# Kernel optimization log

Measured on AMD Instinct MI355X. Metric: run time of the kernel, lower is better.

The kernel has to match this reference:

```python
import jax, jax.numpy as jnp
import numpy as np

POOL = 2  # pool_size from init_kwargs


def setup_inputs() -> dict:
    key = jax.random.key(0)
    b, n = 8192, 64
    A = jax.random.normal(key, (b, n, n), dtype=jnp.float32)
    # SPD construction: A A^T / n + I  (well-conditioned, distinct eigvals a.s.)
    X = A @ jnp.swapaxes(A, -1, -2) / n + jnp.eye(n, dtype=jnp.float32)
    return {"X": X}


def _logm_spd(X):
    # matrix log of batched SPD via eigendecomposition (SPDTangentSpace)
    w, V = jnp.linalg.eigh(X)
    return (V * jnp.log(w)[..., None, :]) @ jnp.swapaxes(V, -1, -2)


def _expm_sym(H):
    # matrix exp of batched symmetric matrices (SPDUnTangentSpace)
    w, V = jnp.linalg.eigh(H)
    return (V * jnp.exp(w)[..., None, :]) @ jnp.swapaxes(V, -1, -2)


def reference(X):
    # log map to tangent space
    logX = _logm_spd(X)
    b, n, _ = logX.shape
    m = n // POOL
    # avg_pool2d(kernel=POOL, stride=POOL) over the (n, n) matrix dims
    pooled = logX.reshape(b, m, POOL, m, POOL).mean(axis=(2, 4))
    # pooling of a symmetric matrix with this block pattern stays symmetric;
    # symmetrize for numerical safety before eigh-based exp map
    pooled = 0.5 * (pooled + jnp.swapaxes(pooled, -1, -2))
    return _expm_sym(pooled)
```

## Files before the change

kernel.cpp:

```cpp
#include <hip/hip_runtime.h>

typedef __attribute__((ext_vector_type(8))) short short8;
typedef __attribute__((ext_vector_type(16))) float f32x16;

#define PL 8192
#define PP0 0
#define PP1 8192
#define PP2 16384
#define PP3 24576
#define PP4 32768

__device__ __forceinline__ int swadr(int m, int kc) {
  return m * 128 + ((kc ^ (m & 7)) << 4);
}

__device__ __forceinline__ unsigned int cvtpk(float a, float b) {
  unsigned int r;
  asm("v_cvt_pk_bf16_f32 %0, %1, %2" : "=v"(r) : "v"(a), "v"(b));
  return r;
}
__device__ __forceinline__ float dppswap(float v) {
  return __int_as_float(
      __builtin_amdgcn_mov_dpp(__float_as_int(v), 0xB1, 0xF, 0xF, true));
}
__device__ __forceinline__ f32x16 zero16() {
  f32x16 z;
#pragma unroll
  for (int i = 0; i < 16; ++i) z[i] = 0.f;
  return z;
}
__device__ __forceinline__ void q16x16(f32x16& v) {
#pragma unroll
  for (int r = 0; r < 16; r += 2) {
    unsigned w = cvtpk(v[r], v[r + 1]);
    v[r] = __uint_as_float(w << 16);
    v[r + 1] = __uint_as_float(w & 0xFFFF0000u);
  }
}

__device__ __forceinline__ void store_hi8(char* dst, const float* v) {
  *(uint4*)dst = make_uint4(cvtpk(v[0], v[1]), cvtpk(v[2], v[3]),
                            cvtpk(v[4], v[5]), cvtpk(v[6], v[7]));
}
__device__ __forceinline__ void split_store8(char* dst, const float* v) {
  unsigned h[4], l[4];
#pragma unroll
  for (int j = 0; j < 4; ++j) {
    unsigned hw = cvtpk(v[2 * j], v[2 * j + 1]);
    float h0 = __uint_as_float(hw << 16);
    float h1 = __uint_as_float(hw & 0xFFFF0000u);
    l[j] = cvtpk(v[2 * j] - h0, v[2 * j + 1] - h1);
    h[j] = hw;
  }
  *(uint4*)dst = make_uint4(h[0], h[1], h[2], h[3]);
  *(uint4*)(dst + PL) = make_uint4(l[0], l[1], l[2], l[3]);
}

template <int NK, int OA, int OB, int N>
__device__ __forceinline__ void mac1(f32x16& acc, char* const (&pA)[N],
                                     char* const (&pB)[N]) {
#pragma unroll
  for (int s = 0; s < NK; ++s) {
    short8 a = *(const short8*)(pA[s] + OA);
    short8 b = *(const short8*)(pB[s] + OB);
    acc = __builtin_amdgcn_mfma_f32_32x32x16_bf16(a, b, acc, 0, 0, 0);
  }
}
template <int NK, int OA, int OB, int N>
__device__ __forceinline__ void mac2A(f32x16& acc, char* const (&pA)[N],
                                      char* const (&pB)[N]) {
#pragma unroll
  for (int s = 0; s < NK; ++s) {
    short8 ah = *(const short8*)(pA[s] + OA);
    short8 al = *(const short8*)(pA[s] + OA + PL);
    short8 b = *(const short8*)(pB[s] + OB);
    acc = __builtin_amdgcn_mfma_f32_32x32x16_bf16(ah, b, acc, 0, 0, 0);
    acc = __builtin_amdgcn_mfma_f32_32x32x16_bf16(al, b, acc, 0, 0, 0);
  }
}
template <int NK, int OA, int OB, int N>
__device__ __forceinline__ void mac2B(f32x16& acc, char* const (&pA)[N],
                                      char* const (&pB)[N]) {
#pragma unroll
  for (int s = 0; s < NK; ++s) {
    short8 a = *(const short8*)(pA[s] + OA);
    short8 bh = *(const short8*)(pB[s] + OB);
    short8 bl = *(const short8*)(pB[s] + OB + PL);
    acc = __builtin_amdgcn_mfma_f32_32x32x16_bf16(a, bh, acc, 0, 0, 0);
    acc = __builtin_amdgcn_mfma_f32_32x32x16_bf16(a, bl, acc, 0, 0, 0);
  }
}
template <int NK, int OA, int OB, int N>
__device__ __forceinline__ void mac3(f32x16& acc, char* const (&pA)[N],
                                     char* const (&pB)[N]) {
#pragma unroll
  for (int s = 0; s < NK; ++s) {
    short8 ah = *(const short8*)(pA[s] + OA);
    short8 al = *(const short8*)(pA[s] + OA + PL);
    short8 bh = *(const short8*)(pB[s] + OB);
    short8 bl = *(const short8*)(pB[s] + OB + PL);
    acc = __builtin_amdgcn_mfma_f32_32x32x16_bf16(ah, bh, acc, 0, 0, 0);
    acc = __builtin_amdgcn_mfma_f32_32x32x16_bf16(ah, bl, acc, 0, 0, 0);
    acc = __builtin_amdgcn_mfma_f32_32x32x16_bf16(al, bh, acc, 0, 0, 0);
  }
}

template <int OFF>
__device__ __forceinline__ void write_hi(char* lds, const int (&wo)[16], bool ev,
                                         const f32x16& vals) {
#pragma unroll
  for (int r = 0; r < 16; ++r) {
    float vn = dppswap(vals[r]);
    unsigned hw = cvtpk(vals[r], vn);
    if (ev) *(unsigned*)(lds + OFF + wo[r]) = hw;
  }
}
template <int OFF>
__device__ __forceinline__ void write_split(char* lds, const int (&wo)[16],
                                            bool ev, int pl, const f32x16& vals,
                                            int r0, int r1) {
#pragma unroll
  for (int r = 0; r < 16; ++r) {
    if (r < r0 || r >= r1) continue;
    float v = vals[r];
    float vn = dppswap(v);
    unsigned hw = cvtpk(v, vn);
    float lo = v - __uint_as_float(hw << 16);
    float lon = dppswap(lo);
    unsigned lw = cvtpk(lon, lo);
    *(unsigned*)(lds + OFF + pl + wo[r]) = ev ? hw : lw;
  }
}

__global__ void __launch_bounds__(256, 4)
spd_pool_kernel(const float* __restrict__ X, float* __restrict__ out) {
  __shared__ __align__(16) char lds[5 * 8192];

  const int tid = threadIdx.x;
  const int lane = tid & 63;
  const int wv = tid >> 6;
  const int R = (wv >> 1) * 32;
  const int Cc = (wv & 1) * 32;
  const int half = lane >> 5;
  const int ln31 = lane & 31;
  const bool ev = (ln31 & 1) == 0;
  const int pl = ev ? 0 : PL;

  char* pA[4];
  char* pB[4];
#pragma unroll
  for (int s = 0; s < 4; ++s) {
    const int kc = 2 * s + half;
    pA[s] = lds + swadr(R + ln31, kc);
    pB[s] = lds + swadr(Cc + ln31, kc);
  }
  int wo[16];
  {
    const int col0 = Cc + (ln31 & ~1);
    const int cchunk = col0 >> 3, cbyte = (col0 & 7) * 2;
    const int rbase = R + 4 * half;
#pragma unroll
    for (int r = 0; r < 16; ++r) {
      const int m = rbase + (r & 3) + 8 * (r >> 2);
      wo[r] = m * 128 + ((cchunk ^ (m & 7)) << 4) + cbyte;
    }
  }
  f32x16 dmask;
#pragma unroll
  for (int r = 0; r < 16; ++r)
    dmask[r] = (R + (r & 3) + 8 * (r >> 2) + 4 * half == Cc + ln31) ? 1.f : 0.f;

  f32x16 mY, mZ;

  {
    const int em = tid >> 2;
    const int ekc = (tid & 3) * 2;
    const int ec0 = ekc * 8;
    const float ic1 = 1.0f / 6.6f;
    const float* Xg = X + (size_t)blockIdx.x * 4096 + em * 64 + ec0;
    const float4* xp = (const float4*)Xg;
    float4 a = xp[0], b = xp[1], c = xp[2], d = xp[3];
    float v[16] = {a.x * ic1, a.y * ic1, a.z * ic1, a.w * ic1,
                   b.x * ic1, b.y * ic1, b.z * ic1, b.w * ic1,
                   c.x * ic1, c.y * ic1, c.z * ic1, c.w * ic1,
                   d.x * ic1, d.y * ic1, d.z * ic1, d.w * ic1};
    float t[16];
#pragma unroll
    for (int i = 0; i < 16; ++i)
      t[i] = ((em == ec0 + i) ? 1.5f : 0.f) - 0.5f * v[i];
    split_store8(lds + PP0 + swadr(em, ekc), v);
    split_store8(lds + PP0 + swadr(em, ekc + 1), v + 8);
    store_hi8(lds + PP2 + swadr(em, ekc), t);
    store_hi8(lds + PP2 + swadr(em, ekc + 1), t + 8);
  }
  __syncthreads();
  mY = zero16();
  mac1<4, PP0, PP2>(mY, pA, pB);
  write_hi<PP3>(lds, wo, ev, mY);
  __syncthreads();
#pragma unroll 1
  for (int it = 0; it < 4; ++it) {
    f32x16 a;
#pragma unroll
    for (int r = 0; r < 16; ++r) a[r] = -3.f * dmask[r];
    mac1<4, PP2, PP3>(a, pA, pB);
    f32x16 tv;
#pragma unroll
    for (int r = 0; r < 16; ++r) tv[r] = -0.5f * a[r];
    write_hi<PP4>(lds, wo, ev, tv);
    __syncthreads();
    mY = zero16();
    mac1<4, PP3, PP4>(mY, pA, pB);
    mZ = zero16();
    mac1<4, PP4, PP2>(mZ, pA, pB);
    __syncthreads();
    write_hi<PP3>(lds, wo, ev, mY);
    write_hi<PP2>(lds, wo, ev, mZ);
    __syncthreads();
  }
  mY = zero16();
  mac2A<4, PP0, PP2>(mY, pA, pB);
  write_split<PP3>(lds, wo, ev, pl, mY, 0, 16);
  __syncthreads();
  {
    f32x16 a;
#pragma unroll
    for (int r = 0; r < 16; ++r) a[r] = -dmask[r];
    mac2B<4, PP2, PP3>(a, pA, pB);
    f32x16 dv;
#pragma unroll
    for (int r = 0; r < 16; ++r) dv[r] = -0.5f * a[r];
    write_hi<PP0>(lds, wo, ev, dv);
  }
  __syncthreads();
  mac1<4, PP3, PP0>(mY, pA, pB);
  __syncthreads();
  write_split<PP3>(lds, wo, ev, pl, mY, 0, 16);
  {
    f32x16 t0v;
#pragma unroll
    for (int r = 0; r < 16; ++r) t0v[r] = 1.5f * dmask[r] - 0.5f * mY[r];
    write_hi<PP2>(lds, wo, ev, t0v);
  }
  __syncthreads();
  mY = zero16();
  mac1<4, PP3, PP2>(mY, pA, pB);
  write_hi<PP0>(lds, wo, ev, mY);
  __syncthreads();
#pragma unroll 1
  for (int it = 0; it < 2; ++it) {
    f32x16 a;
#pragma unroll
    for (int r = 0; r < 16; ++r) a[r] = -3.f * dmask[r];
    mac1<4, PP2, PP0>(a, pA, pB);
    f32x16 tv;
#pragma unroll
    for (int r = 0; r < 16; ++r) tv[r] = -0.5f * a[r];
    write_hi<PP1>(lds, wo, ev, tv);
    __syncthreads();
    mY = zero16();
    mac1<4, PP0, PP1>(mY, pA, pB);
    mZ = zero16();
    mac1<4, PP1, PP2>(mZ, pA, pB);
    __syncthreads();
    write_hi<PP0>(lds, wo, ev, mY);
    write_hi<PP2>(lds, wo, ev, mZ);
    __syncthreads();
  }
  q16x16(mZ);
  mY = zero16();
  mac2A<4, PP3, PP2>(mY, pA, pB);
  write_split<PP0>(lds, wo, ev, pl, mY, 0, 16);
  __syncthreads();
  {
    f32x16 a;
#pragma unroll
    for (int r = 0; r < 16; ++r) a[r] = -dmask[r];
    mac2B<4, PP2, PP0>(a, pA, pB);
    f32x16 dv;
#pragma unroll
    for (int r = 0; r < 16; ++r) dv[r] = -0.5f * a[r];
    write_hi<PP3>(lds, wo, ev, dv);
  }
  __syncthreads();
  mac1<4, PP0, PP3>(mY, pA, pB);
  mac1<4, PP3, PP2>(mZ, pA, pB);
  __syncthreads();
  write_split<PP0>(lds, wo, ev, pl, mY, 0, 16);
  q16x16(mZ);
  write_hi<PP2>(lds, wo, ev, mZ);
  __syncthreads();
  {
    f32x16 a;
#pragma unroll
    for (int r = 0; r < 16; ++r) a[r] = -dmask[r];
    mac2B<4, PP2, PP0>(a, pA, pB);
    f32x16 dv;
#pragma unroll
    for (int r = 0; r < 16; ++r) dv[r] = -0.5f * a[r];
    write_hi<PP3>(lds, wo, ev, dv);
  }
  __syncthreads();
  mac1<4, PP0, PP3>(mY, pA, pB);
  mac1<4, PP3, PP2>(mZ, pA, pB);
  f32x16 sv;
  {
    const float ca = 0.80141224f;
    const float cb = 0.31194493f;
#pragma unroll
    for (int r = 0; r < 16; ++r) sv[r] = ca * mY[r] - cb * mZ[r];
  }
  __syncthreads();
  write_split<PP0>(lds, wo, ev, pl, sv, 0, 16);
  __syncthreads();
  {
    f32x16 s2 = zero16();
    mac3<4, PP0, PP0>(s2, pA, pB);
    const float A11 = -0.08948864f, A9 = 0.12152778f;
    f32x16 qv;
#pragma unroll
    for (int r = 0; r < 16; ++r) qv[r] = A11 * s2[r] + A9 * dmask[r];
    write_hi<PP2>(lds, wo, ev, s2);
    write_hi<PP3>(lds, wo, ev, qv);
  }
  __syncthreads();
  {
    const float acoef[3] = {-0.17857143f, 0.3f, -0.66666667f};
#pragma unroll 1
    for (int j = 0; j < 3; ++j) {
      f32x16 a;
#pragma unroll
      for (int r = 0; r < 16; ++r) a[r] = acoef[j] * dmask[r];
      mac1<4, PP3, PP2>(a, pA, pB);
      __syncthreads();
      write_hi<PP3>(lds, wo, ev, a);
      __syncthreads();
    }
  }
  {
    f32x16 a;
#pragma unroll
    for (int r = 0; r < 16; ++r) a[r] = 4.f * dmask[r];
    mac1<4, PP3, PP2>(a, pA, pB);
    __syncthreads();
    write_split<PP3>(lds, wo, ev, pl, a, 0, 16);
    __syncthreads();
  }
  {
    f32x16 mL = zero16();
    mac3<4, PP0, PP3>(mL, pA, pB);
    __syncthreads();
    const float d8 = 2.4801587e-5f, d7 = 1.9841270e-4f;
#pragma unroll
    for (int q = 0; q < 8; ++q) {
      float rp = mL[2 * q] + mL[2 * q + 1];
      float cs = rp + dppswap(rp);
      float p = 0.125f * cs;
      const int row = R / 2 + (q & 1) + 4 * (q >> 1) + 2 * half;
      const int col = Cc / 2 + (ln31 >> 1);
      float qv = d8 * p + ((row == col) ? d7 : 0.f);
      unsigned phw = cvtpk(p, p);
      float plo = p - __uint_as_float(phw << 16);
      unsigned plw = cvtpk(plo, plo);
      unsigned qhw = cvtpk(qv, qv);
      float qlo = qv - __uint_as_float(qhw << 16);
      unsigned qlw = cvtpk(qlo, qlo);
      const int off = row * 128 + (((col >> 3) ^ (row & 7)) << 4) + (col & 7) * 2;
      if (ev) {
        *(short*)(lds + PP0 + off) = (short)phw;
        *(short*)(lds + PP1 + off) = (short)plw;
        *(short*)(lds + PP2 + off) = (short)qhw;
        *(short*)(lds + PP3 + off) = (short)qlw;
      }
    }
  }
  __syncthreads();
  char* pE[2];
#pragma unroll
  for (int s = 0; s < 2; ++s) pE[s] = lds + swadr(ln31, 2 * s + half);
  f32x16 dmask2;
#pragma unroll
  for (int r = 0; r < 16; ++r)
    dmask2[r] = ((r & 3) + 8 * (r >> 2) + 4 * half == ln31) ? 1.f : 0.f;
  int wo2[16];
  {
    const int col0 = ln31 & ~1;
    const int cchunk = col0 >> 3, cbyte = (col0 & 7) * 2;
    const int rbase = 4 * half;
#pragma unroll
    for (int r = 0; r < 16; ++r) {
      const int m = rbase + (r & 3) + 8 * (r >> 2);
      wo2[r] = m * 128 + ((cchunk ^ (m & 7)) << 4) + cbyte;
    }
  }
  {
    const float dcoef[7] = {1.f / 720.f, 1.f / 120.f, 1.f / 24.f,
                            1.f / 6.f,   0.5f,        1.f,       1.f};
#pragma unroll 1
    for (int j = 0; j < 7; ++j) {
      f32x16 acc;
#pragma unroll
      for (int r = 0; r < 16; ++r) acc[r] = dcoef[j] * dmask2[r];
      mac3<2, PP2, PP0>(acc, pE, pE);
      __syncthreads();
      write_split<PP2>(lds, wo2, ev, pl, acc, 4 * wv, 4 * wv + 4);
      __syncthreads();
    }
  }
  {
    f32x16 acc = zero16();
    mac3<2, PP2, PP2>(acc, pE, pE);
    float* og = out + (size_t)blockIdx.x * 1024;
#pragma unroll
    for (int r = 0; r < 16; ++r) {
      if (r < 4 * wv || r >= 4 * wv + 4) continue;
      int rl = (r & 3) + 8 * (r >> 2) + 4 * half;
      og[rl * 32 + ln31] = acc[r];
    }
  }
}

extern "C" void kernel_launch(void* const* d_in, const int* in_sizes, int n_in,
                              void* d_out, int out_size, void* d_ws, size_t ws_size,
                              hipStream_t stream) {
  const float* X = (const float*)d_in[0];
  float* out = (float*)d_out;
  const int batch = in_sizes[0] / 4096;
  spd_pool_kernel<<<batch, 256, 0, stream>>>(X, out);
}
```

Before: 491.6 us.

## Evaluate exp Taylor polynomial via Paterson-Stockmeyer instead of Horner

Replaces the 7-step Horner evaluation of the degree-8 exp Taylor polynomial on the pooled 32x32 matrix with a Paterson-Stockmeyer scheme. It computes X^2, X^3 and X^4 and combines them as X^4*A + B. This cuts the sequential matrix multiplies and barrier-separated LDS round-trips from about seven to four, followed by the final squaring. The trade-off is extra register pressure from holding several power matrices, plus a slightly different rounding order.

```diff
diff --git a/kernel.cpp b/kernel.cpp
--- a/kernel.cpp
+++ b/kernel.cpp
@@ -350,27 +350,20 @@
     f32x16 mL = zero16();
     mac3<4, PP0, PP3>(mL, pA, pB);
     __syncthreads();
-    const float d8 = 2.4801587e-5f, d7 = 1.9841270e-4f;
 #pragma unroll
     for (int q = 0; q < 8; ++q) {
       float rp = mL[2 * q] + mL[2 * q + 1];
-      float cs = rp + dppswap(rp);
-      float p = 0.125f * cs;
-      const int row = R / 2 + (q & 1) + 4 * (q >> 1) + 2 * half;
-      const int col = Cc / 2 + (ln31 >> 1);
-      float qv = d8 * p + ((row == col) ? d7 : 0.f);
+      float p = 0.125f * (rp + dppswap(rp));
+      const int row = (R >> 1) + (q & 1) + 4 * (q >> 1) + 2 * half;
+      const int colP = (Cc >> 1) + (ln31 >> 1);
       unsigned phw = cvtpk(p, p);
       float plo = p - __uint_as_float(phw << 16);
       unsigned plw = cvtpk(plo, plo);
-      unsigned qhw = cvtpk(qv, qv);
-      float qlo = qv - __uint_as_float(qhw << 16);
-      unsigned qlw = cvtpk(qlo, qlo);
-      const int off = row * 128 + (((col >> 3) ^ (row & 7)) << 4) + (col & 7) * 2;
       if (ev) {
+        const int off =
+            row * 128 + (((colP >> 3) ^ (row & 7)) << 4) + (colP & 7) * 2;
         *(short*)(lds + PP0 + off) = (short)phw;
         *(short*)(lds + PP1 + off) = (short)plw;
-        *(short*)(lds + PP2 + off) = (short)qhw;
-        *(short*)(lds + PP3 + off) = (short)qlw;
       }
     }
   }
@@ -393,19 +386,52 @@
       wo2[r] = m * 128 + ((cchunk ^ (m & 7)) << 4) + cbyte;
     }
   }
-  {
-    const float dcoef[7] = {1.f / 720.f, 1.f / 120.f, 1.f / 24.f,
-                            1.f / 6.f,   0.5f,        1.f,       1.f};
-#pragma unroll 1
-    for (int j = 0; j < 7; ++j) {
-      f32x16 acc;
-#pragma unroll
-      for (int r = 0; r < 16; ++r) acc[r] = dcoef[j] * dmask2[r];
-      mac3<2, PP2, PP0>(acc, pE, pE);
-      __syncthreads();
-      write_split<PP2>(lds, wo2, ev, pl, acc, 4 * wv, 4 * wv + 4);
-      __syncthreads();
-    }
+  const int r0 = 4 * wv, r1 = 4 * wv + 4;
+  {
+    f32x16 x2a = zero16();
+    mac3<2, PP0, PP0>(x2a, pE, pE);
+    f32x16 xsv;
+#pragma unroll
+    for (int r = 0; r < 16; ++r) {
+      xsv[r] = 0.f;
+      if ((r >> 2) == wv) {
+        const int rl = (r & 3) + 8 * (r >> 2) + 4 * half;
+        const int off =
+            rl * 128 + (((ln31 >> 3) ^ (rl & 7)) << 4) + (ln31 & 7) * 2;
+        unsigned hb = *(const unsigned short*)(lds + PP0 + off);
+        unsigned lb = *(const unsigned short*)(lds + PP1 + off);
+        xsv[r] = __uint_as_float(hb << 16) + __uint_as_float(lb << 16);
+      }
+    }
+    write_split<PP2>(lds, wo2, ev, pl, x2a, r0, r1);
+    __syncthreads();
+    f32x16 x3a = zero16();
+    mac3<2, PP2, PP0>(x3a, pE, pE);
+    f32x16 x4a = zero16();
+    mac3<2, PP2, PP2>(x4a, pE, pE);
+    const float c8 = 2.4801587e-5f;
+    const float c7 = 1.9841270e-4f;
+    const float c6 = 1.3888889e-3f;
+    const float c5 = 8.3333333e-3f;
+    const float c4 = 4.1666667e-2f;
+    f32x16 Ac, Bc;
+#pragma unroll
+    for (int r = 0; r < 16; ++r) {
+      Ac[r] = c8 * x4a[r] + c7 * x3a[r] + c6 * x2a[r] + c5 * xsv[r] +
+              c4 * dmask2[r];
+      Bc[r] = 0.16666667f * x3a[r] + 0.5f * x2a[r] + xsv[r] + dmask2[r];
+    }
+    __syncthreads();
+    write_split<PP0>(lds, wo2, ev, pl, x4a, r0, r1);
+    write_split<PP2>(lds, wo2, ev, pl, Ac, r0, r1);
+    __syncthreads();
+    f32x16 Ha = zero16();
+    mac3<2, PP2, PP0>(Ha, pE, pE);
+#pragma unroll
+    for (int r = 0; r < 16; ++r) Ha[r] += Bc[r];
+    __syncthreads();
+    write_split<PP2>(lds, wo2, ev, pl, Ha, r0, r1);
+    __syncthreads();
   }
   {
     f32x16 acc = zero16();
@@ -413,7 +439,7 @@
     float* og = out + (size_t)blockIdx.x * 1024;
 #pragma unroll
     for (int r = 0; r < 16; ++r) {
-      if (r < 4 * wv || r >= 4 * wv + 4) continue;
+      if (r < r0 || r >= r1) continue;
       int rl = (r & 3) + 8 * (r >> 2) + 4 * half;
       og[rl * 32 + ln31] = acc[r];
     }
```

After: 481.2 us. -2.1%, faster.
